# Performance work log

Hardware: AMD Instinct MI355X
Metric: run time of the kernel (lower is better)

The kernel has to match this reference:

```python
import jax, jax.numpy as jnp
import numpy as np

B, L, D, H = 4, 1024, 1024, 16
DH = D // H
NEG = -1e9
EPS = 1e-5


def setup_inputs() -> dict:
    key = jax.random.key(0)
    ks = jax.random.split(key, 12)
    s = 1.0 / np.sqrt(D)
    inp = {
        "Q": jax.random.normal(ks[0], (B, L, D), jnp.float32),
        "K": jax.random.normal(ks[1], (B, L, D), jnp.float32),
        "V": jax.random.normal(ks[2], (B, L, D), jnp.float32),
        "K_mask": jnp.ones((B, L), jnp.int32),
        "WQ": jax.random.normal(ks[3], (D, D), jnp.float32) * s,
        "bQ": jnp.zeros((D,), jnp.float32),
        "WK": jax.random.normal(ks[4], (D, D), jnp.float32) * s,
        "bK": jnp.zeros((D,), jnp.float32),
        "WV": jax.random.normal(ks[5], (D, D), jnp.float32) * s,
        "bV": jnp.zeros((D,), jnp.float32),
        "WO": jax.random.normal(ks[6], (D, D), jnp.float32) * s,
        "bO": jnp.zeros((D,), jnp.float32),
        "ln_g": jnp.ones((D,), jnp.float32),
        "ln_b": jnp.zeros((D,), jnp.float32),
    }
    return inp


def _mha(Q, K, V, K_mask, WQ, bQ, WK, bK, WV, bV, WO, bO, ln_g, ln_b):
    # projections  [B,L,D]
    q = Q @ WQ + bQ
    k = K @ WK + bK
    v = V @ WV + bV
    # split heads -> [B,H,L,dh]
    q = q.reshape(B, L, H, DH).transpose(0, 2, 1, 3)
    k = k.reshape(B, L, H, DH).transpose(0, 2, 1, 3)
    v = v.reshape(B, L, H, DH).transpose(0, 2, 1, 3)
    # scaled dot product, masked softmax over keys
    scores = jnp.einsum("bhqd,bhkd->bhqk", q, k) / jnp.sqrt(jnp.float32(DH))
    mask = (K_mask > 0)[:, None, None, :]  # [B,1,1,Lk]
    scores = jnp.where(mask, scores, NEG)
    attn = jax.nn.softmax(scores, axis=-1)  # dropout is identity at inference
    ctx = jnp.einsum("bhqk,bhkd->bhqd", attn, v)
    ctx = ctx.transpose(0, 2, 1, 3).reshape(B, L, D)
    # output layer: dense + residual + layernorm
    out = ctx @ WO + bO
    x = out + Q
    mu = jnp.mean(x, axis=-1, keepdims=True)
    var = jnp.var(x, axis=-1, keepdims=True)
    return (x - mu) * jax.lax.rsqrt(var + EPS) * ln_g + ln_b


def reference(Q, K, V, K_mask, WQ, bQ, WK, bK, WV, bV, WO, bO, ln_g, ln_b):
    return _mha(Q, K, V, K_mask, WQ, bQ, WK, bK, WV, bV, WO, bO, ln_g, ln_b)
```

## Files before the change

kernel.cpp:

```cpp
#include <hip/hip_runtime.h>
#include <hip/hip_bf16.h>
#include <stdint.h>

#define Bn 4
#define Ln 1024
#define Dn 1024
#define Hn 16
#define DHn 64
#define Mn (Bn*Ln)

typedef __attribute__((ext_vector_type(8))) short short8v;
typedef __attribute__((ext_vector_type(4))) float floatx4;

__device__ __forceinline__ unsigned short f2b(float f){
  union { float f; unsigned u; } v; v.f = f;
  unsigned r = (v.u + 0x7FFFu + ((v.u >> 16) & 1u)) >> 16;
  return (unsigned short)r;
}
__device__ __forceinline__ unsigned short f2b_fast(float f){
  __hip_bfloat16 h = __float2bfloat16(f);
  return *reinterpret_cast<unsigned short*>(&h);
}

typedef const unsigned __attribute__((address_space(1)))* gas1_t;
typedef unsigned __attribute__((address_space(3)))* las3_t;
__device__ __forceinline__ void gload16(const void* g, void* l){
  __builtin_amdgcn_global_load_lds((gas1_t)(uintptr_t)g, (las3_t)(uintptr_t)l, 16, 0, 0);
}

__global__ __launch_bounds__(256) void tobf16x3_k(const float* __restrict__ x0,
    const float* __restrict__ x1, const float* __restrict__ x2,
    unsigned short* __restrict__ o0, unsigned short* __restrict__ o1,
    unsigned short* __restrict__ o2)
{
  const int i = blockIdx.x * 256 + threadIdx.x;
  const int sel = i >> 20, idx = i & 0xFFFFF;
  const float* x = sel == 0 ? x0 : (sel == 1 ? x1 : x2);
  unsigned short* o = sel == 0 ? o0 : (sel == 1 ? o1 : o2);
  float4 v = reinterpret_cast<const float4*>(x)[idx];
  union { unsigned short u[4]; uint2 q; } p;
  p.u[0] = f2b(v.x); p.u[1] = f2b(v.y); p.u[2] = f2b(v.z); p.u[3] = f2b(v.w);
  reinterpret_cast<uint2*>(o)[idx] = p.q;
}

__global__ __launch_bounds__(256) void wconv4_k(const float* __restrict__ W0,
    const float* __restrict__ W1, const float* __restrict__ W2,
    const float* __restrict__ W3, unsigned short* __restrict__ Wt0,
    unsigned short* __restrict__ Wt1, unsigned short* __restrict__ Wt2,
    unsigned short* __restrict__ Wt3)
{
  const float* W; unsigned short* Wt;
  switch (blockIdx.z){
    case 0: W = W0; Wt = Wt0; break;
    case 1: W = W1; Wt = Wt1; break;
    case 2: W = W2; Wt = Wt2; break;
    default: W = W3; Wt = Wt3; break;
  }
  __shared__ float tile[64][65];
  const int nb = blockIdx.x * 64, kb = blockIdx.y * 64;
  const int tx = threadIdx.x & 63, ty = threadIdx.x >> 6;
  #pragma unroll
  for (int r = 0; r < 64; r += 4)
    tile[r + ty][tx] = W[(size_t)(kb + r + ty) * 1024 + nb + tx];
  __syncthreads();
  #pragma unroll
  for (int r = 0; r < 64; r += 4)
    Wt[(size_t)(nb + r + ty) * 1024 + kb + tx] = f2b(tile[tx][r + ty]);
}

template<int MODE>
__device__ __forceinline__ void gemm_core(const unsigned short* __restrict__ Ab,
    const unsigned short* __restrict__ Btp, const float* __restrict__ bias,
    void* __restrict__ outp, const float* __restrict__ resid, float scale,
    unsigned short* lds, int nt, int mt)
{
  unsigned short* ldsA = lds;
  unsigned short* ldsB = lds + 8192;
  const int tid = threadIdx.x;
  const int lane = tid & 63, wave = tid >> 6;
  const int wr = wave >> 1, wc = wave & 1;
  const int lg = lane >> 4, lr = lane & 15;
  const int m0 = mt * 128, n0 = nt * 128;

  const unsigned short* gA[4];
  const unsigned short* gB[4];
  #pragma unroll
  for (int i = 0; i < 4; i++){
    int c = (wave * 4 + i) * 64 + lane;
    int ks = c >> 9, r16 = (c >> 6) & 7, lhi = (c >> 4) & 3, lrr = c & 15;
    int row = r16 * 16 + lrr, col = ks * 32 + lhi * 8;
    gA[i] = Ab  + (size_t)(m0 + row) * 1024 + col;
    gB[i] = Btp + (size_t)(n0 + row) * 1024 + col;
  }

  floatx4 acc[4][4] = {};

  for (int kb = 0; kb < 16; kb++){
    if (kb) __syncthreads();
    #pragma unroll
    for (int i = 0; i < 4; i++){
      gload16(gA[i] + kb * 64, &ldsA[(wave * 4 + i) * 512]);
      gload16(gB[i] + kb * 64, &ldsB[(wave * 4 + i) * 512]);
    }
    asm volatile("s_waitcnt vmcnt(0)" ::: "memory");
    __syncthreads();
    #pragma unroll
    for (int ks = 0; ks < 2; ks++){
      short8v af[4], bfr[4];
      #pragma unroll
      for (int m = 0; m < 4; m++)
        af[m] = *reinterpret_cast<const short8v*>(&ldsA[((ks * 8 + wr * 4 + m) * 64 + lane) * 8]);
      #pragma unroll
      for (int n = 0; n < 4; n++)
        bfr[n] = *reinterpret_cast<const short8v*>(&ldsB[((ks * 8 + wc * 4 + n) * 64 + lane) * 8]);
      #pragma unroll
      for (int m = 0; m < 4; m++)
        #pragma unroll
        for (int n = 0; n < 4; n++)
          acc[m][n] = __builtin_amdgcn_mfma_f32_16x16x32_bf16(af[m], bfr[n], acc[m][n], 0, 0, 0);
    }
  }

  if constexpr (MODE == 2){
    __syncthreads();
    #pragma unroll
    for (int n = 0; n < 4; n++){
      const int gn_l = wc * 64 + n * 16 + lr;
      const float bb = bias[n0 + gn_l];
      const int X = (gn_l & 7) << 3;
      #pragma unroll
      for (int m = 0; m < 4; m++){
        const int gm_l = wr * 64 + m * 16 + lg * 4;
        union { unsigned short u[4]; uint2 q; } pk;
        #pragma unroll
        for (int r = 0; r < 4; r++) pk.u[r] = f2b((acc[m][n][r] + bb) * scale);
        *reinterpret_cast<uint2*>(&lds[gn_l * 128 + (gm_l ^ X)]) = pk.q;
      }
    }
    __syncthreads();
    const int b = m0 >> 10, l0 = m0 & 1023;
    const int row = tid >> 1, colb = (tid & 1) * 64;
    const int h2 = (n0 + row) >> 6, d = (n0 + row) & 63;
    unsigned short* obase = (unsigned short*)outp +
        (((size_t)(b * Hn + h2)) * DHn + d) * Ln + l0 + colb;
    const int XR = (row & 7) << 3;
    #pragma unroll
    for (int g = 0; g < 8; g++){
      short8v v = *reinterpret_cast<const short8v*>(&lds[row * 128 + ((colb + g * 8) ^ XR)]);
      *reinterpret_cast<short8v*>(obase + g * 8) = v;
    }
  } else {
    #pragma unroll
    for (int n = 0; n < 4; n++){
      const int gn = n0 + wc * 64 + n * 16 + lr;
      const float bb = bias[gn];
      #pragma unroll
      for (int m = 0; m < 4; m++){
        const int gm0 = m0 + wr * 64 + m * 16 + lg * 4;
        #pragma unroll
        for (int r = 0; r < 4; r++){
          const int gm = gm0 + r;
          float v = (acc[m][n][r] + bb) * scale;
          if constexpr (MODE == 0){
            unsigned short* o = (unsigned short*)outp;
            int b = gm >> 10, l = gm & 1023, h2 = gn >> 6, d = gn & 63;
            o[(((size_t)(b * Hn + h2)) * Ln + l) * DHn + d] = f2b(v);
          } else {
            float* o = (float*)outp;
            o[(size_t)gm * Dn + gn] = v + resid[(size_t)gm * Dn + gn];
          }
        }
      }
    }
  }
}

__global__ __launch_bounds__(256) void gemmqkv_k(
    const unsigned short* __restrict__ A0, const unsigned short* __restrict__ A1,
    const unsigned short* __restrict__ A2, const unsigned short* __restrict__ W0,
    const unsigned short* __restrict__ W1, const unsigned short* __restrict__ W2,
    const float* __restrict__ b0, const float* __restrict__ b1,
    const float* __restrict__ b2, unsigned short* __restrict__ o0,
    unsigned short* __restrict__ o1, unsigned short* __restrict__ o2, float qscl)
{
  __shared__ __align__(16) unsigned short lds[16384];
  const int bid = blockIdx.x;
  const int xcd = bid & 7, k = bid >> 3;
  const int panel = (k >> 3) * 8 + xcd;
  const int nt = k & 7;
  const int mt = panel & 31, z = panel >> 5;
  if (z == 0)
    gemm_core<0>(A0, W0, b0, o0, nullptr, qscl, lds, nt, mt);
  else if (z == 1)
    gemm_core<0>(A1, W1, b1, o1, nullptr, 1.f, lds, nt, mt);
  else
    gemm_core<2>(A2, W2, b2, o2, nullptr, 1.f, lds, nt, mt);
}

__global__ __launch_bounds__(256) void gemmo_k(const unsigned short* __restrict__ Ab,
    const unsigned short* __restrict__ W, const float* __restrict__ bias,
    float* __restrict__ out, const float* __restrict__ resid)
{
  __shared__ __align__(16) unsigned short lds[16384];
  const int bid = blockIdx.x;
  const int xcd = bid & 7, k = bid >> 3;
  const int mt = (k >> 3) * 8 + xcd;
  const int nt = k & 7;
  gemm_core<3>(Ab, W, bias, out, resid, 1.f, lds, nt, mt);
}

__global__ __launch_bounds__(256) void attn_k(const unsigned short* __restrict__ qb,
    const unsigned short* __restrict__ kbf, const unsigned short* __restrict__ vtb,
    const int* __restrict__ kmask, unsigned short* __restrict__ ctx)
{
  const int bh = blockIdx.x;
  const int qt = blockIdx.y;
  const int b = bh >> 4, h = bh & 15;
  const int tid = threadIdx.x;
  const int w = tid >> 6, lane = tid & 63;
  const int lg = lane >> 4, lr = lane & 15;

  const unsigned short* qp = qb  + (size_t)bh * Ln * DHn;
  const unsigned short* kp = kbf + (size_t)bh * Ln * DHn;
  const unsigned short* vp = vtb + (size_t)bh * DHn * Ln;
  const int q0 = qt * 128 + w * 32;

  __shared__ __align__(16) unsigned short ldsK[2][4096];
  __shared__ __align__(16) unsigned short ldsV[2][4096];
  __shared__ __align__(16) unsigned short plds[4][32][72];

  const unsigned short* gK[2];
  const unsigned short* gV[2];
  #pragma unroll
  for (int i = 0; i < 2; i++){
    int bc = w * 2 + i;
    int ks = bc >> 2, j = bc & 3;
    int row = j * 16 + lr, col = ks * 32 + lg * 8;
    gK[i] = kp + (size_t)row * DHn + col;
    gV[i] = vp + (size_t)row * Ln  + col;
  }

  short8v aq[2][2];
  #pragma unroll
  for (int f = 0; f < 2; f++)
    #pragma unroll
    for (int ks = 0; ks < 2; ks++)
      aq[f][ks] = *reinterpret_cast<const short8v*>(
          qp + (size_t)(q0 + f * 16 + lr) * DHn + ks * 32 + lg * 8);

  floatx4 accO[2][4] = {};
  float lsacc[2][4] = {{0.f,0.f,0.f,0.f},{0.f,0.f,0.f,0.f}};

  const int* mrow = kmask + b * Ln;
  int mkA[4], mkB[4];

  #pragma unroll
  for (int i = 0; i < 2; i++){
    gload16(gK[i], &ldsK[0][(w * 2 + i) * 512]);
    gload16(gV[i], &ldsV[0][(w * 2 + i) * 512]);
  }
  #pragma unroll
  for (int j = 0; j < 4; j++) mkA[j] = mrow[j * 16 + lr];

  for (int t = 0; t < 16; t++){
    const int cur = t & 1;
    asm volatile("s_waitcnt vmcnt(0)" ::: "memory");
    __syncthreads();
    if (t < 15){
      #pragma unroll
      for (int i = 0; i < 2; i++){
        gload16(gK[i] + (size_t)(t + 1) * 4096, &ldsK[cur ^ 1][(w * 2 + i) * 512]);
        gload16(gV[i] + (size_t)(t + 1) * 64,   &ldsV[cur ^ 1][(w * 2 + i) * 512]);
      }
      #pragma unroll
      for (int j = 0; j < 4; j++) mkB[j] = mrow[(t + 1) * 64 + j * 16 + lr];
    }

    floatx4 s[2][4] = {};
    #pragma unroll
    for (int ks = 0; ks < 2; ks++)
      #pragma unroll
      for (int j = 0; j < 4; j++){
        short8v bk = *reinterpret_cast<const short8v*>(&ldsK[cur][((ks * 4 + j) * 64 + lane) * 8]);
        s[0][j] = __builtin_amdgcn_mfma_f32_16x16x32_bf16(aq[0][ks], bk, s[0][j], 0, 0, 0);
        s[1][j] = __builtin_amdgcn_mfma_f32_16x16x32_bf16(aq[1][ks], bk, s[1][j], 0, 0, 0);
      }
    if (__all(mkA[0] > 0 && mkA[1] > 0 && mkA[2] > 0 && mkA[3] > 0)){
      #pragma unroll
      for (int f = 0; f < 2; f++)
        #pragma unroll
        for (int j = 0; j < 4; j++)
          #pragma unroll
          for (int r = 0; r < 4; r++){
            float p = __builtin_amdgcn_exp2f(s[f][j][r]);
            lsacc[f][r] += p;
            plds[w][f * 16 + lg * 4 + r][j * 16 + lr] = f2b_fast(p);
          }
    } else {
      #pragma unroll
      for (int j = 0; j < 4; j++){
        const float madd = mkA[j] > 0 ? 0.f : -1e9f;
        #pragma unroll
        for (int f = 0; f < 2; f++)
          #pragma unroll
          for (int r = 0; r < 4; r++){
            float p = __builtin_amdgcn_exp2f(s[f][j][r] + madd);
            lsacc[f][r] += p;
            plds[w][f * 16 + lg * 4 + r][j * 16 + lr] = f2b_fast(p);
          }
      }
    }
    #pragma unroll
    for (int ks = 0; ks < 2; ks++){
      short8v pa0 = *reinterpret_cast<const short8v*>(&plds[w][lr][ks * 32 + lg * 8]);
      short8v pa1 = *reinterpret_cast<const short8v*>(&plds[w][16 + lr][ks * 32 + lg * 8]);
      #pragma unroll
      for (int n = 0; n < 4; n++){
        short8v bv = *reinterpret_cast<const short8v*>(&ldsV[cur][((ks * 4 + n) * 64 + lane) * 8]);
        accO[0][n] = __builtin_amdgcn_mfma_f32_16x16x32_bf16(pa0, bv, accO[0][n], 0, 0, 0);
        accO[1][n] = __builtin_amdgcn_mfma_f32_16x16x32_bf16(pa1, bv, accO[1][n], 0, 0, 0);
      }
    }
    #pragma unroll
    for (int j = 0; j < 4; j++) mkA[j] = mkB[j];
  }

  #pragma unroll
  for (int f = 0; f < 2; f++)
    #pragma unroll
    for (int r = 0; r < 4; r++){
      lsacc[f][r] += __shfl_xor(lsacc[f][r], 1, 64);
      lsacc[f][r] += __shfl_xor(lsacc[f][r], 2, 64);
      lsacc[f][r] += __shfl_xor(lsacc[f][r], 4, 64);
      lsacc[f][r] += __shfl_xor(lsacc[f][r], 8, 64);
      lsacc[f][r] = 1.f / fmaxf(lsacc[f][r], 1e-20f);
    }
  #pragma unroll
  for (int f = 0; f < 2; f++)
    #pragma unroll
    for (int n = 0; n < 4; n++)
      #pragma unroll
      for (int r = 0; r < 4; r++){
        float o = accO[f][n][r] * lsacc[f][r];
        int q = q0 + f * 16 + lg * 4 + r;
        ctx[((size_t)(b * Ln + q)) * Dn + h * DHn + n * 16 + lr] = f2b_fast(o);
      }
}

__global__ __launch_bounds__(256) void ln_k(const float* __restrict__ x,
    const float* __restrict__ g, const float* __restrict__ bt, float* __restrict__ out)
{
  const int row = blockIdx.x;
  const int tid = threadIdx.x;
  float4 v = *reinterpret_cast<const float4*>(x + (size_t)row * 1024 + tid * 4);
  float s  = v.x + v.y + v.z + v.w;
  float sq = v.x * v.x + v.y * v.y + v.z * v.z + v.w * v.w;
  #pragma unroll
  for (int off = 32; off >= 1; off >>= 1){
    s  += __shfl_xor(s, off, 64);
    sq += __shfl_xor(sq, off, 64);
  }
  __shared__ float psm[4], pqm[4];
  const int w = tid >> 6;
  if ((tid & 63) == 0){ psm[w] = s; pqm[w] = sq; }
  __syncthreads();
  s  = psm[0] + psm[1] + psm[2] + psm[3];
  sq = pqm[0] + pqm[1] + pqm[2] + pqm[3];
  const float mean = s * (1.f / 1024.f);
  const float var  = sq * (1.f / 1024.f) - mean * mean;
  const float inv  = rsqrtf(var + 1e-5f);
  float4 gg = *reinterpret_cast<const float4*>(g  + tid * 4);
  float4 bb = *reinterpret_cast<const float4*>(bt + tid * 4);
  float4 o;
  o.x = (v.x - mean) * inv * gg.x + bb.x;
  o.y = (v.y - mean) * inv * gg.y + bb.y;
  o.z = (v.z - mean) * inv * gg.z + bb.z;
  o.w = (v.w - mean) * inv * gg.w + bb.w;
  *reinterpret_cast<float4*>(out + (size_t)row * 1024 + tid * 4) = o;
}

extern "C" void kernel_launch(void* const* d_in, const int* in_sizes, int n_in,
                              void* d_out, int out_size, void* d_ws, size_t ws_size,
                              hipStream_t stream)
{
  const float* Qin = (const float*)d_in[0];
  const float* Kin = (const float*)d_in[1];
  const float* Vin = (const float*)d_in[2];
  const int*   Kms = (const int*)d_in[3];
  const float* WQ  = (const float*)d_in[4];
  const float* bQ  = (const float*)d_in[5];
  const float* WK  = (const float*)d_in[6];
  const float* bK  = (const float*)d_in[7];
  const float* WV  = (const float*)d_in[8];
  const float* bV  = (const float*)d_in[9];
  const float* WO  = (const float*)d_in[10];
  const float* bO  = (const float*)d_in[11];
  const float* lng = (const float*)d_in[12];
  const float* lnb = (const float*)d_in[13];

  char* ws = (char*)d_ws;
  const size_t MB = 1024u * 1024u;
  unsigned short* wqt = (unsigned short*)(ws + 0 * MB);
  unsigned short* wkt = (unsigned short*)(ws + 2 * MB);
  unsigned short* wvt = (unsigned short*)(ws + 4 * MB);
  unsigned short* wot = (unsigned short*)(ws + 6 * MB);
  unsigned short* qbf = (unsigned short*)(ws + 8 * MB);
  unsigned short* kbf = (unsigned short*)(ws + 16 * MB);
  unsigned short* vtb = (unsigned short*)(ws + 24 * MB);
  unsigned short* ctx = (unsigned short*)(ws + 32 * MB);
  float*          xbf = (float*)(ws + 40 * MB);
  unsigned short* cv0 = (unsigned short*)(ws + 32 * MB);
  unsigned short* cv1 = (unsigned short*)(ws + 40 * MB);
  unsigned short* cv2 = (unsigned short*)(ws + 48 * MB);

  dim3 blk(256);
  wconv4_k<<<dim3(16, 16, 4), blk, 0, stream>>>(WQ, WK, WV, WO, wqt, wkt, wvt, wot);
  tobf16x3_k<<<12288, blk, 0, stream>>>(Qin, Kin, Vin, cv0, cv1, cv2);

  const float QSCL = 0.125f * 1.44269504088896f;
  gemmqkv_k<<<768, blk, 0, stream>>>(cv0, cv1, cv2, wqt, wkt, wvt,
                                     bQ, bK, bV, qbf, kbf, vtb, QSCL);

  attn_k<<<dim3(64, 8), blk, 0, stream>>>(qbf, kbf, vtb, Kms, ctx);

  gemmo_k<<<256, blk, 0, stream>>>(ctx, wot, bO, xbf, Qin);

  ln_k<<<4096, blk, 0, stream>>>(xbf, lng, lnb, (float*)d_out);
}
```

Baseline: 143.3 us.

## Use per-wave private LDS double buffering in GEMM core without block barriers

The GEMM main loop now gives each wave its own LDS region holding only the A rows and B columns it consumes. The loop double-buffers in 32-wide k steps, prefetching the next slice with direct global-to-LDS loads and waiting with vmcnt(8) instead of block-wide __syncthreads. This removes the block barriers and overlaps loads with MFMA work. The cost is redundant global loads, since waves sharing the same rows or columns each fetch their own copy, LDS doubles to 64KB per block (which may lower occupancy), and the main loop runs twice as many iterations.

New measurement: 182.9 us. +27.7%, slower.

```diff
diff --git a/kernel.cpp b/kernel.cpp
--- a/kernel.cpp
+++ b/kernel.cpp
@@ -74,51 +74,57 @@
     void* __restrict__ outp, const float* __restrict__ resid, float scale,
     unsigned short* lds, int nt, int mt)
 {
-  unsigned short* ldsA = lds;
-  unsigned short* ldsB = lds + 8192;
   const int tid = threadIdx.x;
   const int lane = tid & 63, wave = tid >> 6;
   const int wr = wave >> 1, wc = wave & 1;
   const int lg = lane >> 4, lr = lane & 15;
   const int m0 = mt * 128, n0 = nt * 128;
 
+  unsigned short* wlds = lds + wave * 8192;
+
   const unsigned short* gA[4];
   const unsigned short* gB[4];
   #pragma unroll
-  for (int i = 0; i < 4; i++){
-    int c = (wave * 4 + i) * 64 + lane;
-    int ks = c >> 9, r16 = (c >> 6) & 7, lhi = (c >> 4) & 3, lrr = c & 15;
-    int row = r16 * 16 + lrr, col = ks * 32 + lhi * 8;
-    gA[i] = Ab  + (size_t)(m0 + row) * 1024 + col;
-    gB[i] = Btp + (size_t)(n0 + row) * 1024 + col;
+  for (int c = 0; c < 4; c++){
+    gA[c] = Ab  + (size_t)(m0 + wr * 64 + c * 16 + lr) * 1024 + lg * 8;
+    gB[c] = Btp + (size_t)(n0 + wc * 64 + c * 16 + lr) * 1024 + lg * 8;
   }
 
   floatx4 acc[4][4] = {};
 
-  for (int kb = 0; kb < 16; kb++){
-    if (kb) __syncthreads();
-    #pragma unroll
-    for (int i = 0; i < 4; i++){
-      gload16(gA[i] + kb * 64, &ldsA[(wave * 4 + i) * 512]);
-      gload16(gB[i] + kb * 64, &ldsB[(wave * 4 + i) * 512]);
-    }
-    asm volatile("s_waitcnt vmcnt(0)" ::: "memory");
-    __syncthreads();
-    #pragma unroll
-    for (int ks = 0; ks < 2; ks++){
-      short8v af[4], bfr[4];
-      #pragma unroll
-      for (int m = 0; m < 4; m++)
-        af[m] = *reinterpret_cast<const short8v*>(&ldsA[((ks * 8 + wr * 4 + m) * 64 + lane) * 8]);
+  #pragma unroll
+  for (int c = 0; c < 4; c++){
+    gload16(gA[c], &wlds[c * 512]);
+    gload16(gB[c], &wlds[2048 + c * 512]);
+  }
+
+  for (int h = 0; h < 32; h++){
+    const int cur = (h & 1) * 4096;
+    if (h < 31){
+      const int nxt = 4096 - cur;
+      const int off = (h + 1) * 32;
+      #pragma unroll
+      for (int c = 0; c < 4; c++){
+        gload16(gA[c] + off, &wlds[nxt + c * 512]);
+        gload16(gB[c] + off, &wlds[nxt + 2048 + c * 512]);
+      }
+      asm volatile("s_waitcnt vmcnt(8)" ::: "memory");
+    } else {
+      asm volatile("s_waitcnt vmcnt(0)" ::: "memory");
+    }
+    __builtin_amdgcn_sched_barrier(0);
+    short8v af[4], bf[4];
+    #pragma unroll
+    for (int m = 0; m < 4; m++)
+      af[m] = *reinterpret_cast<const short8v*>(&wlds[cur + (m * 64 + lane) * 8]);
+    #pragma unroll
+    for (int n = 0; n < 4; n++)
+      bf[n] = *reinterpret_cast<const short8v*>(&wlds[cur + 2048 + (n * 64 + lane) * 8]);
+    #pragma unroll
+    for (int m = 0; m < 4; m++)
       #pragma unroll
       for (int n = 0; n < 4; n++)
-        bfr[n] = *reinterpret_cast<const short8v*>(&ldsB[((ks * 8 + wc * 4 + n) * 64 + lane) * 8]);
-      #pragma unroll
-      for (int m = 0; m < 4; m++)
-        #pragma unroll
-        for (int n = 0; n < 4; n++)
-          acc[m][n] = __builtin_amdgcn_mfma_f32_16x16x32_bf16(af[m], bfr[n], acc[m][n], 0, 0, 0);
-    }
+        acc[m][n] = __builtin_amdgcn_mfma_f32_16x16x32_bf16(af[m], bf[n], acc[m][n], 0, 0, 0);
   }
 
   if constexpr (MODE == 2){
@@ -183,7 +189,7 @@
     const float* __restrict__ b2, unsigned short* __restrict__ o0,
     unsigned short* __restrict__ o1, unsigned short* __restrict__ o2, float qscl)
 {
-  __shared__ __align__(16) unsigned short lds[16384];
+  __shared__ __align__(16) unsigned short lds[32768];
   const int bid = blockIdx.x;
   const int xcd = bid & 7, k = bid >> 3;
   const int panel = (k >> 3) * 8 + xcd;
@@ -201,7 +207,7 @@
     const unsigned short* __restrict__ W, const float* __restrict__ bias,
     float* __restrict__ out, const float* __restrict__ resid)
 {
-  __shared__ __align__(16) unsigned short lds[16384];
+  __shared__ __align__(16) unsigned short lds[32768];
   const int bid = blockIdx.x;
   const int xcd = bid & 7, k = bid >> 3;
   const int mt = (k >> 3) * 8 + xcd;
```

## Triple-buffer GEMM K-loop with async prefetch and remap tiles per XCD

Applied to the files above, without the earlier changes.

Turns the single-buffered GEMM main loop into a three-stage LDS ring. Global-to-LDS loads for tile kb+2 are issued while tile kb is being computed, with partial vmcnt waits and raw s_barriers replacing the full drain and __syncthreads every iteration. It also changes the block-to-tile mapping so each XCD handles a contiguous run of M panels, which should improve L2 reuse. The cost is three times the LDS per block (96KB), which may cut occupancy to one block per CU.

Result: faster. 137.5 us (-4.0%).

```diff
diff --git a/kernel.cpp b/kernel.cpp
--- a/kernel.cpp
+++ b/kernel.cpp
@@ -74,8 +74,6 @@
     void* __restrict__ outp, const float* __restrict__ resid, float scale,
     unsigned short* lds, int nt, int mt)
 {
-  unsigned short* ldsA = lds;
-  unsigned short* ldsB = lds + 8192;
   const int tid = threadIdx.x;
   const int lane = tid & 63, wave = tid >> 6;
   const int wr = wave >> 1, wc = wave & 1;
@@ -95,30 +93,49 @@
 
   floatx4 acc[4][4] = {};
 
+  auto issue = [&](int t){
+    unsigned short* bufA = lds + (t % 3) * 16384;
+    unsigned short* bufB = bufA + 8192;
+    #pragma unroll
+    for (int i = 0; i < 4; i++){
+      gload16(gA[i] + t * 64, &bufA[(wave * 4 + i) * 512]);
+      gload16(gB[i] + t * 64, &bufB[(wave * 4 + i) * 512]);
+    }
+  };
+
+  issue(0);
+  issue(1);
+
   for (int kb = 0; kb < 16; kb++){
-    if (kb) __syncthreads();
-    #pragma unroll
-    for (int i = 0; i < 4; i++){
-      gload16(gA[i] + kb * 64, &ldsA[(wave * 4 + i) * 512]);
-      gload16(gB[i] + kb * 64, &ldsB[(wave * 4 + i) * 512]);
-    }
-    asm volatile("s_waitcnt vmcnt(0)" ::: "memory");
-    __syncthreads();
+    unsigned short* bufA = lds + (kb % 3) * 16384;
+    unsigned short* bufB = bufA + 8192;
+    if (kb < 14){
+      issue(kb + 2);
+      asm volatile("s_waitcnt vmcnt(16)" ::: "memory");
+    } else if (kb == 14){
+      asm volatile("s_waitcnt vmcnt(8)" ::: "memory");
+    } else {
+      asm volatile("s_waitcnt vmcnt(0)" ::: "memory");
+    }
+    __builtin_amdgcn_s_barrier();
+    __builtin_amdgcn_sched_barrier(0);
     #pragma unroll
     for (int ks = 0; ks < 2; ks++){
       short8v af[4], bfr[4];
       #pragma unroll
       for (int m = 0; m < 4; m++)
-        af[m] = *reinterpret_cast<const short8v*>(&ldsA[((ks * 8 + wr * 4 + m) * 64 + lane) * 8]);
+        af[m] = *reinterpret_cast<const short8v*>(&bufA[((ks * 8 + wr * 4 + m) * 64 + lane) * 8]);
       #pragma unroll
       for (int n = 0; n < 4; n++)
-        bfr[n] = *reinterpret_cast<const short8v*>(&ldsB[((ks * 8 + wc * 4 + n) * 64 + lane) * 8]);
+        bfr[n] = *reinterpret_cast<const short8v*>(&bufB[((ks * 8 + wc * 4 + n) * 64 + lane) * 8]);
       #pragma unroll
       for (int m = 0; m < 4; m++)
         #pragma unroll
         for (int n = 0; n < 4; n++)
           acc[m][n] = __builtin_amdgcn_mfma_f32_16x16x32_bf16(af[m], bfr[n], acc[m][n], 0, 0, 0);
     }
+    __builtin_amdgcn_sched_barrier(0);
+    __builtin_amdgcn_s_barrier();
   }
 
   if constexpr (MODE == 2){
@@ -183,10 +200,10 @@
     const float* __restrict__ b2, unsigned short* __restrict__ o0,
     unsigned short* __restrict__ o1, unsigned short* __restrict__ o2, float qscl)
 {
-  __shared__ __align__(16) unsigned short lds[16384];
+  __shared__ __align__(16) unsigned short lds[49152];
   const int bid = blockIdx.x;
   const int xcd = bid & 7, k = bid >> 3;
-  const int panel = (k >> 3) * 8 + xcd;
+  const int panel = xcd * 12 + (k >> 3);
   const int nt = k & 7;
   const int mt = panel & 31, z = panel >> 5;
   if (z == 0)
@@ -201,10 +218,10 @@
     const unsigned short* __restrict__ W, const float* __restrict__ bias,
     float* __restrict__ out, const float* __restrict__ resid)
 {
-  __shared__ __align__(16) unsigned short lds[16384];
+  __shared__ __align__(16) unsigned short lds[49152];
   const int bid = blockIdx.x;
   const int xcd = bid & 7, k = bid >> 3;
-  const int mt = (k >> 3) * 8 + xcd;
+  const int mt = xcd * 4 + (k >> 3);
   const int nt = k & 7;
   gemm_core<3>(Ab, W, bias, out, resid, 1.f, lds, nt, mt);
 }
```
